# Kernel tuning notes

Hardware: AMD Instinct MI355X
Metric: run time of the kernel (lower is better)

The kernel has to match this reference:

```python
import jax, jax.numpy as jnp
import numpy as np

N_NODES = 50000
N_EDGES = 600000
IN_CH = 128
OUT_CH = 64
HID = 2 * OUT_CH  # 128


def setup_inputs() -> dict:
    key = jax.random.key(0)
    k1, k2, k3, k4 = jax.random.split(key, 4)
    x = jax.random.normal(k1, (N_NODES, IN_CH), dtype=jnp.float32)
    edge_index = jax.random.randint(k2, (2, N_EDGES), 0, N_NODES, dtype=jnp.int64)
    # Glorot-style init scale for linear weights (PyG GCNConv default init)
    W1 = jax.random.normal(k3, (IN_CH, HID), dtype=jnp.float32) * (1.0 / np.sqrt(IN_CH))
    b1 = jnp.zeros((HID,), dtype=jnp.float32)
    W2 = jax.random.normal(k4, (HID, OUT_CH), dtype=jnp.float32) * (1.0 / np.sqrt(HID))
    b2 = jnp.zeros((OUT_CH,), dtype=jnp.float32)
    return {"x": x, "edge_index": edge_index, "W1": W1, "b1": b1, "W2": W2, "b2": b2}


def _gcn_norm(edge_index, n_nodes):
    # Add self loops, then symmetric normalization: norm_e = d^-1/2[src] * d^-1/2[dst]
    loop = jnp.arange(n_nodes, dtype=edge_index.dtype)
    src = jnp.concatenate([edge_index[0], loop])
    dst = jnp.concatenate([edge_index[1], loop])
    deg = jax.ops.segment_sum(jnp.ones_like(dst, dtype=jnp.float32), dst, num_segments=n_nodes)
    dinv = jnp.where(deg > 0, jax.lax.rsqrt(deg), 0.0)
    norm = dinv[src] * dinv[dst]  # [E + N]
    return src, dst, norm


def _gcn_conv(x, src, dst, norm, W, b, n_nodes):
    h = x @ W                      # [N, d_out]  dense transform first (PyG order)
    msg = h[src] * norm[:, None]   # gather + scale: [E+N, d_out]
    agg = jax.ops.segment_sum(msg, dst, num_segments=n_nodes)  # scatter-add
    return agg + b


def reference(x, edge_index, W1, b1, W2, b2):
    n = x.shape[0]
    src, dst, norm = _gcn_norm(edge_index, n)  # shared (cached=True in original)
    h = jax.nn.relu(_gcn_conv(x, src, dst, norm, W1, b1, n))
    return _gcn_conv(h, src, dst, norm, W2, b2, n)
```

## Files before the change

kernel.cpp:

```cpp
#include <hip/hip_runtime.h>


typedef __attribute__((ext_vector_type(8))) short short8;
typedef __attribute__((ext_vector_type(4))) float float4v;

constexpr int PB = 128;

static __device__ __forceinline__ ushort f2bf(float f) {
  union { float f; unsigned u; } c; c.f = f;
  unsigned u = c.u;
  return (ushort)((u + 0x7fffu + ((u >> 16) & 1u)) >> 16);
}
static __device__ __forceinline__ float bf2f(ushort h) {
  union { unsigned u; float f; } c; c.u = ((unsigned)h) << 16;
  return c.f;
}
static __device__ __forceinline__ float bfhi(unsigned packed) {
  union { unsigned u; float f; } c; c.u = packed & 0xffff0000u;
  return c.f;
}
static __device__ __forceinline__ float bflo(unsigned packed) {
  union { unsigned u; float f; } c; c.u = packed << 16;
  return c.f;
}

struct MegaParams {
  const float* x;
  const int* src;
  const int* dst;
  const float* W1;
  const float* b1;
  const float* W2;
  const float* b2;
  int N, E, NBK, EPB, GB, NAGG;
  int* cnt_mat;
  int* bases;
  unsigned* part;
  int* row_ptr;
  float* dinv;
  int* col;
  ushort* h;
  ushort* h1hi;
  ushort* h1lo;
  ushort* h2;
  ushort* w1hi;
  ushort* w1lo;
  ushort* w2hi;
  ushort* w2lo;
  float* out;
};

static __device__ __forceinline__ void wswz_tile(const float* __restrict__ W,
                                                 ushort* __restrict__ whi,
                                                 ushort* __restrict__ wlo,
                                                 int M, int tile, int lane) {
  int ntiles = M >> 4;
  int kt = tile / ntiles, nt = tile % ntiles;
  int colg = nt * 16 + (lane & 15);
  int krow = kt * 32 + (lane >> 4) * 8;
  size_t o = ((size_t)tile * 64 + lane) * 8;
#pragma unroll
  for (int j = 0; j < 8; j++) {
    float v = W[(size_t)(krow + j) * M + colg];
    ushort h = f2bf(v);
    whi[o + j] = h;
    wlo[o + j] = f2bf(v - bf2f(h));
  }
}

__global__ __launch_bounds__(256) void k_g1(MegaParams P) {
  __shared__ int hist[512];
  int bid = blockIdx.x, t = threadIdx.x;
  if (bid >= PB) {
    int tile = (bid - PB) * 4 + (t >> 6);
    int lane = t & 63;
    if (tile < 32) wswz_tile(P.W1, P.w1hi, P.w1lo, 128, tile, lane);
    else           wswz_tile(P.W2, P.w2hi, P.w2lo, 64, tile - 32, lane);
    return;
  }
  for (int k = t; k < P.NBK; k += 256) hist[k] = 0;
  __syncthreads();
  int start = bid * P.EPB;
  int stop = min(P.E, start + P.EPB);
  for (int e = start + t * 4; e < stop; e += 1024) {
    if (e + 4 <= stop) {
      int4 d = *(const int4*)(P.dst + e);
      atomicAdd(&hist[d.x >> 7], 1);
      atomicAdd(&hist[d.y >> 7], 1);
      atomicAdd(&hist[d.z >> 7], 1);
      atomicAdd(&hist[d.w >> 7], 1);
    } else {
      for (int j = e; j < stop; j++) atomicAdd(&hist[P.dst[j] >> 7], 1);
    }
  }
  __syncthreads();
  for (int k = t; k < P.NBK; k += 256) P.cnt_mat[k * PB + bid] = hist[k];
}

static __device__ void gemm1_block(int gb, const MegaParams& P) {
  constexpr int K = 128, M = 128, NT = M / 16;
  int t = threadIdx.x;
  int lane = t & 63;
  int wv = t >> 6;
  int quad = lane >> 4, lo16 = lane & 15;
  int rowbase = gb * 64 + wv * 16;
  int arow = rowbase + lo16;
  bool arow_ok = arow < P.N;
  float4v acc[NT];
#pragma unroll
  for (int nt = 0; nt < NT; nt++) acc[nt] = (float4v){0.f, 0.f, 0.f, 0.f};
  for (int kt = 0; kt < 4; kt++) {
    short8 ahi, alo;
    float av[8];
    if (arow_ok) {
      const float* ap = P.x + (size_t)arow * K + kt * 32 + quad * 8;
      float4 a0 = *(const float4*)ap;
      float4 a1 = *(const float4*)(ap + 4);
      av[0] = a0.x; av[1] = a0.y; av[2] = a0.z; av[3] = a0.w;
      av[4] = a1.x; av[5] = a1.y; av[6] = a1.z; av[7] = a1.w;
    } else {
#pragma unroll
      for (int j = 0; j < 8; j++) av[j] = 0.f;
    }
#pragma unroll
    for (int j = 0; j < 8; j++) {
      ushort hh = f2bf(av[j]);
      ahi[j] = (short)hh;
      alo[j] = (short)f2bf(av[j] - bf2f(hh));
    }
    const ushort* ph = P.w1hi + ((size_t)(kt * NT) * 64 + lane) * 8;
    const ushort* pl = P.w1lo + ((size_t)(kt * NT) * 64 + lane) * 8;
#pragma unroll
    for (int nt = 0; nt < NT; nt++) {
      short8 bhi = *(const short8*)(ph + nt * 512);
      short8 blo = *(const short8*)(pl + nt * 512);
      acc[nt] = __builtin_amdgcn_mfma_f32_16x16x32_bf16(ahi, bhi, acc[nt], 0, 0, 0);
      acc[nt] = __builtin_amdgcn_mfma_f32_16x16x32_bf16(alo, bhi, acc[nt], 0, 0, 0);
      acc[nt] = __builtin_amdgcn_mfma_f32_16x16x32_bf16(ahi, blo, acc[nt], 0, 0, 0);
    }
  }
#pragma unroll
  for (int nt = 0; nt < NT; nt++) {
#pragma unroll
    for (int r = 0; r < 4; r++) {
      int row = rowbase + quad * 4 + r;
      if (row < P.N) P.h[(size_t)row * M + nt * 16 + lo16] = f2bf(acc[nt][r]);
    }
  }
}

__global__ __launch_bounds__(256) void k_g2(MegaParams P) {
  __shared__ int buf[256];
  __shared__ int base[512];
  __shared__ int tot[512];
  __shared__ int cur[512];
  int bid = blockIdx.x, t = threadIdx.x;
  if (bid >= PB) {
    gemm1_block(bid - PB, P);
    return;
  }
  for (int k = t; k < P.NBK; k += 256) {
    const int* row = P.cnt_mat + (size_t)k * PB;
    int pre = 0, s = 0;
    for (int b = 0; b < PB; b++) {
      int c = row[b];
      s += c;
      if (b < bid) pre += c;
    }
    tot[k] = s;
    cur[k] = pre;
  }
  __syncthreads();
  {
    int carry = 0;
    for (int b0 = 0; b0 < 512; b0 += 256) {
      int idx = b0 + t;
      int v = (idx < P.NBK) ? tot[idx] : 0;
      buf[t] = v;
      __syncthreads();
      for (int off = 1; off < 256; off <<= 1) {
        int add = (t >= off) ? buf[t - off] : 0;
        __syncthreads();
        buf[t] += add;
        __syncthreads();
      }
      base[idx] = carry + buf[t] - v;
      carry += buf[255];
      __syncthreads();
    }
  }
  for (int k = t; k < P.NBK; k += 256) cur[k] += base[k];
  if (bid == 0)
    for (int k = t; k <= P.NBK; k += 256) P.bases[k] = base[k];
  __syncthreads();
  int start = bid * P.EPB, stop = min(P.E, start + P.EPB);
  for (int e = start + t * 4; e < stop; e += 1024) {
    if (e + 4 <= stop) {
      int4 s = *(const int4*)(P.src + e);
      int4 d = *(const int4*)(P.dst + e);
      int p;
      p = atomicAdd(&cur[d.x >> 7], 1); P.part[p] = (unsigned)s.x | ((unsigned)(d.x & 127) << 25);
      p = atomicAdd(&cur[d.y >> 7], 1); P.part[p] = (unsigned)s.y | ((unsigned)(d.y & 127) << 25);
      p = atomicAdd(&cur[d.z >> 7], 1); P.part[p] = (unsigned)s.z | ((unsigned)(d.z & 127) << 25);
      p = atomicAdd(&cur[d.w >> 7], 1); P.part[p] = (unsigned)s.w | ((unsigned)(d.w & 127) << 25);
    } else {
      for (int j = e; j < stop; j++) {
        int p2 = atomicAdd(&cur[P.dst[j] >> 7], 1);
        P.part[p2] = (unsigned)P.src[j] | ((unsigned)(P.dst[j] & 127) << 25);
      }
    }
  }
}

__global__ __launch_bounds__(256) void k_g3(MegaParams P) {
  __shared__ int buf[256];
  __shared__ int cnt[128];
  __shared__ int cur[128];
  int bid = blockIdx.x, t = threadIdx.x;
  int beg = P.bases[bid], end = P.bases[bid + 1];
  if (t < 128) cnt[t] = 0;
  __syncthreads();
  for (int e = beg + t; e < end; e += 256) atomicAdd(&cnt[P.part[e] >> 25], 1);
  __syncthreads();
  int v = (t < 128) ? cnt[t] : 0;
  buf[t] = v;
  __syncthreads();
#pragma unroll
  for (int off = 1; off < 256; off <<= 1) {
    int add = (t >= off) ? buf[t - off] : 0;
    __syncthreads();
    buf[t] += add;
    __syncthreads();
  }
  if (t < 128) {
    int excl = buf[t] - v;
    cur[t] = beg + excl;
    int node = bid * 128 + t;
    if (node < P.N) {
      P.row_ptr[node] = beg + excl;
      P.dinv[node] = rsqrtf((float)(v + 1));
    }
  }
  if (bid == 0 && t == 0) P.row_ptr[P.N] = P.E;
  __syncthreads();
  for (int e = beg + t; e < end; e += 256) {
    unsigned p = P.part[e];
    int pos = atomicAdd(&cur[p >> 25], 1);
    P.col[pos] = (int)(p & 0x01FFFFFFu);
  }
}

template <int C, bool RELU, bool SPLIT>
static __device__ void agg_block(int vb, const MegaParams& P,
                                 const ushort* __restrict__ Hb,
                                 const float* __restrict__ bias,
                                 float* __restrict__ out,
                                 ushort* __restrict__ outhi,
                                 ushort* __restrict__ outlo) {
  constexpr int VPL = C / 64;
  int lane = threadIdx.x & 63;
  int v = vb * 4 + (threadIdx.x >> 6);
  if (v >= P.N) return;
  float dv = P.dinv[v];
  float acc0 = 0.f, acc1 = 0.f;
  auto loadp = [&](int s) -> unsigned {
    if (VPL == 2) return *(const unsigned*)(Hb + (size_t)s * C + lane * 2);
    else          return (unsigned)Hb[(size_t)s * C + lane];
  };
  {
    unsigned u = loadp(v);
    if (VPL == 2) { acc0 = dv * bflo(u); acc1 = dv * bfhi(u); }
    else          { acc0 = dv * bf2f((ushort)u); }
  }
  int beg = P.row_ptr[v], end = P.row_ptr[v + 1];
  for (int base = beg; base < end; base += 64) {
    int m = end - base;
    if (m > 64) m = 64;
    int sl = 0;
    float wl = 0.f;
    if (lane < m) {
      sl = P.col[base + lane];
      wl = P.dinv[sl];
    }
    int j = 0;
    for (; j + 8 <= m; j += 8) {
      int s[8]; float wq[8]; unsigned u[8];
#pragma unroll
      for (int q = 0; q < 8; q++) { s[q] = __shfl(sl, j + q); wq[q] = __shfl(wl, j + q); }
#pragma unroll
      for (int q = 0; q < 8; q++) u[q] = loadp(s[q]);
#pragma unroll
      for (int q = 0; q < 8; q++) {
        if (VPL == 2) {
          acc0 = fmaf(wq[q], bflo(u[q]), acc0);
          acc1 = fmaf(wq[q], bfhi(u[q]), acc1);
        } else {
          acc0 = fmaf(wq[q], bf2f((ushort)u[q]), acc0);
        }
      }
    }
    for (; j + 4 <= m; j += 4) {
      int s[4]; float wq[4]; unsigned u[4];
#pragma unroll
      for (int q = 0; q < 4; q++) { s[q] = __shfl(sl, j + q); wq[q] = __shfl(wl, j + q); }
#pragma unroll
      for (int q = 0; q < 4; q++) u[q] = loadp(s[q]);
#pragma unroll
      for (int q = 0; q < 4; q++) {
        if (VPL == 2) {
          acc0 = fmaf(wq[q], bflo(u[q]), acc0);
          acc1 = fmaf(wq[q], bfhi(u[q]), acc1);
        } else {
          acc0 = fmaf(wq[q], bf2f((ushort)u[q]), acc0);
        }
      }
    }
    for (; j < m; j++) {
      int s = __shfl(sl, j);
      float wv = __shfl(wl, j);
      unsigned u = loadp(s);
      if (VPL == 2) {
        acc0 = fmaf(wv, bflo(u), acc0);
        acc1 = fmaf(wv, bfhi(u), acc1);
      } else {
        acc0 = fmaf(wv, bf2f((ushort)u), acc0);
      }
    }
  }
  float r0 = fmaf(dv, acc0, bias[lane * VPL + 0]);
  if (RELU) r0 = fmaxf(r0, 0.f);
  if (VPL == 2) {
    float r1 = fmaf(dv, acc1, bias[lane * VPL + 1]);
    if (RELU) r1 = fmaxf(r1, 0.f);
    if (SPLIT) {
      ushort h0 = f2bf(r0), h1 = f2bf(r1);
      ushort l0 = f2bf(r0 - bf2f(h0)), l1 = f2bf(r1 - bf2f(h1));
      ((unsigned*)outhi)[(size_t)v * (C / 2) + lane] = (unsigned)h0 | ((unsigned)h1 << 16);
      ((unsigned*)outlo)[(size_t)v * (C / 2) + lane] = (unsigned)l0 | ((unsigned)l1 << 16);
    } else {
      *(float2*)&out[(size_t)v * C + lane * 2] = make_float2(r0, r1);
    }
  } else {
    out[(size_t)v * C + lane] = r0;
  }
}

__global__ __launch_bounds__(256) void k_g5(MegaParams P) {
  constexpr int K = 128, M = 64, NT = M / 16;
  int t = threadIdx.x;
  int lane = t & 63;
  int wv = t >> 6;
  int quad = lane >> 4, lo16 = lane & 15;
  int rowbase = blockIdx.x * 64 + wv * 16;
  int arow = rowbase + lo16;
  bool arow_ok = arow < P.N;
  float4v acc[NT];
#pragma unroll
  for (int nt = 0; nt < NT; nt++) acc[nt] = (float4v){0.f, 0.f, 0.f, 0.f};
  for (int kt = 0; kt < 4; kt++) {
    short8 ahi, alo;
    if (arow_ok) {
      size_t ao = (size_t)arow * K + kt * 32 + quad * 8;
      ahi = *(const short8*)(P.h1hi + ao);
      alo = *(const short8*)(P.h1lo + ao);
    } else {
      ahi = (short8)0; alo = (short8)0;
    }
    const ushort* ph = P.w2hi + ((size_t)(kt * NT) * 64 + lane) * 8;
    const ushort* pl = P.w2lo + ((size_t)(kt * NT) * 64 + lane) * 8;
#pragma unroll
    for (int nt = 0; nt < NT; nt++) {
      short8 bhi = *(const short8*)(ph + nt * 512);
      short8 blo = *(const short8*)(pl + nt * 512);
      acc[nt] = __builtin_amdgcn_mfma_f32_16x16x32_bf16(ahi, bhi, acc[nt], 0, 0, 0);
      acc[nt] = __builtin_amdgcn_mfma_f32_16x16x32_bf16(alo, bhi, acc[nt], 0, 0, 0);
      acc[nt] = __builtin_amdgcn_mfma_f32_16x16x32_bf16(ahi, blo, acc[nt], 0, 0, 0);
    }
  }
#pragma unroll
  for (int nt = 0; nt < NT; nt++) {
#pragma unroll
    for (int r = 0; r < 4; r++) {
      int row = rowbase + quad * 4 + r;
      if (row < P.N) P.h2[(size_t)row * M + nt * 16 + lo16] = f2bf(acc[nt][r]);
    }
  }
}

__global__ __launch_bounds__(256) void k_g4(MegaParams P) {
  agg_block<128, true, true>(blockIdx.x, P, P.h, P.b1, nullptr, P.h1hi, P.h1lo);
}
__global__ __launch_bounds__(256) void k_g6(MegaParams P) {
  agg_block<64, false, false>(blockIdx.x, P, P.h2, P.b2, P.out, nullptr, nullptr);
}

extern "C" void kernel_launch(void* const* d_in, const int* in_sizes, int n_in,
                              void* d_out, int out_size, void* d_ws, size_t ws_size,
                              hipStream_t stream) {
  MegaParams P;
  P.x  = (const float*)d_in[0];
  const int* ei = (const int*)d_in[1];
  P.W1 = (const float*)d_in[2];
  P.b1 = (const float*)d_in[3];
  P.W2 = (const float*)d_in[4];
  P.b2 = (const float*)d_in[5];
  P.N = in_sizes[0] / 128;
  P.E = in_sizes[1] / 2;
  P.src = ei;
  P.dst = ei + P.E;
  P.NBK = (P.N + 127) / 128;
  P.EPB = ((P.E + PB - 1) / PB + 3) & ~3;
  P.GB = (P.N + 63) / 64;
  P.NAGG = (P.N + 3) / 4;

  auto al = [](size_t v) { return (v + 255) & ~(size_t)255; };
  char* w = (char*)d_ws;
  P.cnt_mat = (int*)w;      w += al((size_t)P.NBK * PB * 4);
  P.bases   = (int*)w;      w += al((size_t)(P.NBK + 1) * 4);
  P.part    = (unsigned*)w; w += al((size_t)P.E * 4);
  P.row_ptr = (int*)w;      w += al((size_t)(P.N + 1) * 4);
  P.dinv    = (float*)w;    w += al((size_t)P.N * 4);
  P.col     = (int*)w;      w += al((size_t)P.E * 4);
  P.h       = (ushort*)w;   w += al((size_t)P.N * 128 * 2);
  P.h1hi    = (ushort*)w;   w += al((size_t)P.N * 128 * 2);
  P.h1lo    = (ushort*)w;   w += al((size_t)P.N * 128 * 2);
  P.h2      = (ushort*)w;   w += al((size_t)P.N * 64 * 2);
  P.w1hi    = (ushort*)w;   w += al((size_t)128 * 128 * 2);
  P.w1lo    = (ushort*)w;   w += al((size_t)128 * 128 * 2);
  P.w2hi    = (ushort*)w;   w += al((size_t)128 * 64 * 2);
  P.w2lo    = (ushort*)w;   w += al((size_t)128 * 64 * 2);
  P.out = (float*)d_out;

  k_g1<<<PB + 12, 256, 0, stream>>>(P);
  k_g2<<<PB + P.GB, 256, 0, stream>>>(P);
  k_g3<<<P.NBK, 256, 0, stream>>>(P);
  k_g4<<<P.NAGG, 256, 0, stream>>>(P);
  k_g5<<<P.GB, 256, 0, stream>>>(P);
  k_g6<<<P.NAGG, 256, 0, stream>>>(P);
}
```

Measured before the change: 172.0 us.

## Fuse layer-1 aggregation with second GEMM via shared-memory staging

Merges the layer-1 gather/aggregate kernel and the second MFMA GEMM into one kernel: each wave aggregates 16 nodes sequentially, writes the split hi/lo bf16 rows to LDS, then runs the MFMA from LDS. This removes the global write and reread of the split h1 buffers and one launch. In exchange each wave processes nodes serially and the grid becomes much smaller with significant LDS use, reducing parallelism for the latency-bound gather.

```diff
diff --git a/kernel.cpp b/kernel.cpp
--- a/kernel.cpp
+++ b/kernel.cpp
@@ -5,6 +5,7 @@
 typedef __attribute__((ext_vector_type(4))) float float4v;
 
 constexpr int PB = 128;
+constexpr int LDA = 136;
 
 static __device__ __forceinline__ ushort f2bf(float f) {
   union { float f; unsigned u; } c; c.f = f;
@@ -40,8 +41,6 @@
   float* dinv;
   int* col;
   ushort* h;
-  ushort* h1hi;
-  ushort* h1lo;
   ushort* h2;
   ushort* w1hi;
   ushort* w1lo;
@@ -250,19 +249,12 @@
   }
 }
 
-template <int C, bool RELU, bool SPLIT>
-static __device__ void agg_block(int vb, const MegaParams& P,
-                                 const ushort* __restrict__ Hb,
-                                 const float* __restrict__ bias,
-                                 float* __restrict__ out,
-                                 ushort* __restrict__ outhi,
-                                 ushort* __restrict__ outlo) {
+template <int C>
+static __device__ __forceinline__ void agg_node(int v, const MegaParams& P,
+                                                const ushort* __restrict__ Hb,
+                                                int lane, float dv,
+                                                float& acc0, float& acc1) {
   constexpr int VPL = C / 64;
-  int lane = threadIdx.x & 63;
-  int v = vb * 4 + (threadIdx.x >> 6);
-  if (v >= P.N) return;
-  float dv = P.dinv[v];
-  float acc0 = 0.f, acc1 = 0.f;
   auto loadp = [&](int s) -> unsigned {
     if (VPL == 2) return *(const unsigned*)(Hb + (size_t)s * C + lane * 2);
     else          return (unsigned)Hb[(size_t)s * C + lane];
@@ -270,7 +262,7 @@
   {
     unsigned u = loadp(v);
     if (VPL == 2) { acc0 = dv * bflo(u); acc1 = dv * bfhi(u); }
-    else          { acc0 = dv * bf2f((ushort)u); }
+    else          { acc0 = dv * bf2f((ushort)u); acc1 = 0.f; }
   }
   int beg = P.row_ptr[v], end = P.row_ptr[v + 1];
   for (int base = beg; base < end; base += 64) {
@@ -327,45 +319,44 @@
       }
     }
   }
-  float r0 = fmaf(dv, acc0, bias[lane * VPL + 0]);
-  if (RELU) r0 = fmaxf(r0, 0.f);
-  if (VPL == 2) {
-    float r1 = fmaf(dv, acc1, bias[lane * VPL + 1]);
-    if (RELU) r1 = fmaxf(r1, 0.f);
-    if (SPLIT) {
+}
+
+__global__ __launch_bounds__(256) void k_g45(MegaParams P) {
+  __shared__ ushort Ahi[64 * LDA];
+  __shared__ ushort Alo[64 * LDA];
+  int t = threadIdx.x;
+  int lane = t & 63, wv = t >> 6;
+  int nodebase = blockIdx.x * 64 + wv * 16;
+
+  for (int i = 0; i < 16; i++) {
+    int v = nodebase + i;
+    int lrow = wv * 16 + i;
+    unsigned uh = 0, ul = 0;
+    if (v < P.N) {
+      float dv = P.dinv[v];
+      float a0, a1;
+      agg_node<128>(v, P, P.h, lane, dv, a0, a1);
+      float r0 = fmaxf(fmaf(dv, a0, P.b1[lane * 2 + 0]), 0.f);
+      float r1 = fmaxf(fmaf(dv, a1, P.b1[lane * 2 + 1]), 0.f);
       ushort h0 = f2bf(r0), h1 = f2bf(r1);
       ushort l0 = f2bf(r0 - bf2f(h0)), l1 = f2bf(r1 - bf2f(h1));
-      ((unsigned*)outhi)[(size_t)v * (C / 2) + lane] = (unsigned)h0 | ((unsigned)h1 << 16);
-      ((unsigned*)outlo)[(size_t)v * (C / 2) + lane] = (unsigned)l0 | ((unsigned)l1 << 16);
-    } else {
-      *(float2*)&out[(size_t)v * C + lane * 2] = make_float2(r0, r1);
-    }
-  } else {
-    out[(size_t)v * C + lane] = r0;
-  }
-}
-
-__global__ __launch_bounds__(256) void k_g5(MegaParams P) {
+      uh = (unsigned)h0 | ((unsigned)h1 << 16);
+      ul = (unsigned)l0 | ((unsigned)l1 << 16);
+    }
+    *(unsigned*)&Ahi[lrow * LDA + lane * 2] = uh;
+    *(unsigned*)&Alo[lrow * LDA + lane * 2] = ul;
+  }
+
   constexpr int K = 128, M = 64, NT = M / 16;
-  int t = threadIdx.x;
-  int lane = t & 63;
-  int wv = t >> 6;
   int quad = lane >> 4, lo16 = lane & 15;
-  int rowbase = blockIdx.x * 64 + wv * 16;
-  int arow = rowbase + lo16;
-  bool arow_ok = arow < P.N;
   float4v acc[NT];
 #pragma unroll
   for (int nt = 0; nt < NT; nt++) acc[nt] = (float4v){0.f, 0.f, 0.f, 0.f};
   for (int kt = 0; kt < 4; kt++) {
-    short8 ahi, alo;
-    if (arow_ok) {
-      size_t ao = (size_t)arow * K + kt * 32 + quad * 8;
-      ahi = *(const short8*)(P.h1hi + ao);
-      alo = *(const short8*)(P.h1lo + ao);
-    } else {
-      ahi = (short8)0; alo = (short8)0;
-    }
+    int lrow = wv * 16 + lo16;
+    int ko = kt * 32 + quad * 8;
+    short8 ahi = *(const short8*)&Ahi[lrow * LDA + ko];
+    short8 alo = *(const short8*)&Alo[lrow * LDA + ko];
     const ushort* ph = P.w2hi + ((size_t)(kt * NT) * 64 + lane) * 8;
     const ushort* pl = P.w2lo + ((size_t)(kt * NT) * 64 + lane) * 8;
 #pragma unroll
@@ -381,17 +372,20 @@
   for (int nt = 0; nt < NT; nt++) {
 #pragma unroll
     for (int r = 0; r < 4; r++) {
-      int row = rowbase + quad * 4 + r;
+      int row = nodebase + quad * 4 + r;
       if (row < P.N) P.h2[(size_t)row * M + nt * 16 + lo16] = f2bf(acc[nt][r]);
     }
   }
 }
 
-__global__ __launch_bounds__(256) void k_g4(MegaParams P) {
-  agg_block<128, true, true>(blockIdx.x, P, P.h, P.b1, nullptr, P.h1hi, P.h1lo);
-}
 __global__ __launch_bounds__(256) void k_g6(MegaParams P) {
-  agg_block<64, false, false>(blockIdx.x, P, P.h2, P.b2, P.out, nullptr, nullptr);
+  int lane = threadIdx.x & 63;
+  int v = blockIdx.x * 4 + (threadIdx.x >> 6);
+  if (v >= P.N) return;
+  float dv = P.dinv[v];
+  float a0, a1;
+  agg_node<64>(v, P, P.h2, lane, dv, a0, a1);
+  P.out[(size_t)v * 64 + lane] = fmaf(dv, a0, P.b2[lane]);
 }
 
 extern "C" void kernel_launch(void* const* d_in, const int* in_sizes, int n_in,
@@ -422,8 +416,6 @@
   P.dinv    = (float*)w;    w += al((size_t)P.N * 4);
   P.col     = (int*)w;      w += al((size_t)P.E * 4);
   P.h       = (ushort*)w;   w += al((size_t)P.N * 128 * 2);
-  P.h1hi    = (ushort*)w;   w += al((size_t)P.N * 128 * 2);
-  P.h1lo    = (ushort*)w;   w += al((size_t)P.N * 128 * 2);
   P.h2      = (ushort*)w;   w += al((size_t)P.N * 64 * 2);
   P.w1hi    = (ushort*)w;   w += al((size_t)128 * 128 * 2);
   P.w1lo    = (ushort*)w;   w += al((size_t)128 * 128 * 2);
@@ -434,7 +426,6 @@
   k_g1<<<PB + 12, 256, 0, stream>>>(P);
   k_g2<<<PB + P.GB, 256, 0, stream>>>(P);
   k_g3<<<P.NBK, 256, 0, stream>>>(P);
-  k_g4<<<P.NAGG, 256, 0, stream>>>(P);
-  k_g5<<<P.GB, 256, 0, stream>>>(P);
+  k_g45<<<P.GB, 256, 0, stream>>>(P);
   k_g6<<<P.NAGG, 256, 0, stream>>>(P);
 }
```

Result: slower. 179.6 us (+4.4%).
